# Kernel tuning notes

Hardware: AMD Instinct MI355X
Metric: run time of the kernel (lower is better)

## Reference

```python
import jax, jax.numpy as jnp
import numpy as np

B, S, C = 64, 2048, 128
P, Q = 4, 4


def setup_inputs() -> dict:
    key = jax.random.key(0)
    k1, k2, k3 = jax.random.split(key, 3)
    y = jax.random.normal(k1, (B, S, C), dtype=jnp.float32)
    # small positive coefficients keep the MA recurrence stable over S steps
    phi = 0.1 * jax.random.uniform(k2, (P,), dtype=jnp.float32)
    theta = 0.1 * jax.random.uniform(k3, (Q,), dtype=jnp.float32)
    sigma2 = jnp.ones((1,), dtype=jnp.float32)
    return {"y": y, "phi": phi, "theta": theta, "sigma2": sigma2}


def reference(y, phi, theta, sigma2):
    # ARIMA negative log-likelihood (arima_log_likelihood):
    #   e_t = y_t - sum_i phi_i * y_{t-i-1} - sum_j theta_j * e_{t-j-1}
    #   nll = -[ -0.5*S*log(2*pi*sigma2) - 0.5*sum(e^2)/sigma2 ]
    b, s, c = y.shape
    p = phi.shape[0]
    q = theta.shape[0]

    # AR part is a fixed causal convolution over the input -> precompute, vectorized.
    ypad = jnp.pad(y, ((0, 0), (p, 0), (0, 0)))  # zeros for t-i-1 < 0
    # lags[i, :, t, :] = y[:, t-i-1, :]   (zero when out of range)
    lags = jnp.stack([ypad[:, p - 1 - i: p - 1 - i + s, :] for i in range(p)], axis=0)
    z = y - jnp.einsum('i,ibsc->bsc', phi, lags)  # (B,S,C)

    # MA part is a true recurrence on the errors -> lax.scan over time.
    def step(carry, z_t):
        # carry: (q, B, C) = [e_{t-1}, e_{t-2}, ..., e_{t-q}] (most recent first)
        ma = jnp.einsum('j,jbc->bc', theta, carry)
        e_t = z_t - ma
        carry = jnp.concatenate([e_t[None], carry[:-1]], axis=0)
        return carry, e_t

    e0 = jnp.zeros((q, b, c), dtype=z.dtype)
    _, e = jax.lax.scan(step, e0, jnp.swapaxes(z, 0, 1))  # e: (S,B,C)

    ll = -0.5 * s * jnp.log(2.0 * jnp.pi * sigma2) - 0.5 * jnp.sum(e * e) / sigma2
    return -ll  # shape (1,)
```

## Files before the change

kernel.cpp:

```cpp
#include <hip/hip_runtime.h>
#include <math.h>

#define BB   64
#define SS   2048
#define CC   128
#define C4   (CC / 4)
#define LCH  64
#define NCH  (SS / LCH)
#define WARM 32
#define UNR  16
#define STEPS (WARM + LCH)
#define NBLK  (STEPS / UNR)
#define WBLK  (WARM / UNR)

#define ARIMA_BATCH(SRC, ACCT)                                            \
    _Pragma("unroll")                                                     \
    for (int j = 0; j < UNR; ++j) {                                       \
        _Pragma("unroll")                                                 \
        for (int k = 0; k < 4; ++k) {                                     \
            const float y0 = SRC[j][k];                                   \
            const float z  = y0 - p1*Y1[k] - p2*Y2[k] - p3*Y3[k] - p4*Y4[k]; \
            const float e0 = z  - q2*E2[k] - q3*E3[k] - q4*E4[k] - q1*E1[k]; \
            if (ACCT) acc[k] += e0 * e0;                                  \
            Y4[k] = Y3[k]; Y3[k] = Y2[k]; Y2[k] = Y1[k]; Y1[k] = y0;      \
            E4[k] = E3[k]; E3[k] = E2[k]; E2[k] = E1[k]; E1[k] = e0;      \
        }                                                                 \
    }

__global__ __launch_bounds__(64) void arima_main(
    const float4* __restrict__ yv,
    const float* __restrict__ phi,
    const float* __restrict__ theta,
    float* __restrict__ partials)
{
    const int bid  = blockIdx.x;
    const int lane = threadIdx.x;
    const int grp  = lane >> 5;
    const int ch   = lane & 31;
    const int b    = bid >> 4;
    const int chunk = ((bid & 15) << 1) | grp;

    const float p1 = phi[0],   p2 = phi[1],   p3 = phi[2],   p4 = phi[3];
    const float q1 = theta[0], q2 = theta[1], q3 = theta[2], q4 = theta[3];

    const float4* base = yv + (size_t)b * SS * C4 + ch;
    const int t0 = chunk * LCH - WARM;

    float Y1[4] = {0,0,0,0}, Y2[4] = {0,0,0,0}, Y3[4] = {0,0,0,0}, Y4[4] = {0,0,0,0};
    if (t0 >= 4) {
        float4 v;
        v = base[(size_t)(t0-1) * C4]; Y1[0]=v.x; Y1[1]=v.y; Y1[2]=v.z; Y1[3]=v.w;
        v = base[(size_t)(t0-2) * C4]; Y2[0]=v.x; Y2[1]=v.y; Y2[2]=v.z; Y2[3]=v.w;
        v = base[(size_t)(t0-3) * C4]; Y3[0]=v.x; Y3[1]=v.y; Y3[2]=v.z; Y3[3]=v.w;
        v = base[(size_t)(t0-4) * C4]; Y4[0]=v.x; Y4[1]=v.y; Y4[2]=v.z; Y4[3]=v.w;
    }
    float E1[4] = {0,0,0,0}, E2[4] = {0,0,0,0}, E3[4] = {0,0,0,0}, E4[4] = {0,0,0,0};
    float acc[4] = {0,0,0,0};

    int tcur = t0;
    float cur[UNR][4];
#pragma unroll
    for (int j = 0; j < UNR; ++j) {
        const int t = tcur + j;
        float4 v = (t >= 0) ? base[(size_t)t * C4] : make_float4(0.f,0.f,0.f,0.f);
        cur[j][0]=v.x; cur[j][1]=v.y; cur[j][2]=v.z; cur[j][3]=v.w;
    }
    tcur += UNR;

    for (int blk = 0; blk < NBLK - 1; ++blk) {
        float nxt[UNR][4];
#pragma unroll
        for (int j = 0; j < UNR; ++j) {
            const int t = tcur + j;
            float4 v = (t >= 0) ? base[(size_t)t * C4] : make_float4(0.f,0.f,0.f,0.f);
            nxt[j][0]=v.x; nxt[j][1]=v.y; nxt[j][2]=v.z; nxt[j][3]=v.w;
        }
        tcur += UNR;
        const bool acct = (blk >= WBLK);
        ARIMA_BATCH(cur, acct)
#pragma unroll
        for (int j = 0; j < UNR; ++j) {
            cur[j][0]=nxt[j][0]; cur[j][1]=nxt[j][1];
            cur[j][2]=nxt[j][2]; cur[j][3]=nxt[j][3];
        }
    }
    ARIMA_BATCH(cur, true)

    float a = acc[0] + acc[1] + acc[2] + acc[3];
#pragma unroll
    for (int off = 32; off > 0; off >>= 1)
        a += __shfl_down(a, off, 64);
    if (lane == 0) partials[bid] = a;
}

__global__ __launch_bounds__(256) void arima_final(
    const float* __restrict__ partials,
    const float* __restrict__ sigma2,
    float* __restrict__ out)
{
    float v = 0.f;
#pragma unroll
    for (int i = 0; i < 4; ++i)
        v += partials[threadIdx.x + 256 * i];
#pragma unroll
    for (int off = 32; off > 0; off >>= 1)
        v += __shfl_down(v, off, 64);
    __shared__ float sw[4];
    if ((threadIdx.x & 63) == 0) sw[threadIdx.x >> 6] = v;
    __syncthreads();
    if (threadIdx.x == 0) {
        const float tot = sw[0] + sw[1] + sw[2] + sw[3];
        const float s2 = sigma2[0];
        out[0] = 0.5f * (float)SS * logf(2.0f * 3.14159265358979323846f * s2)
               + 0.5f * tot / s2;
    }
}

extern "C" void kernel_launch(void* const* d_in, const int* in_sizes, int n_in,
                              void* d_out, int out_size, void* d_ws, size_t ws_size,
                              hipStream_t stream) {
    const float4* yv    = (const float4*)d_in[0];
    const float* phi    = (const float*)d_in[1];
    const float* theta  = (const float*)d_in[2];
    const float* sigma2 = (const float*)d_in[3];
    float* out      = (float*)d_out;
    float* partials = (float*)d_ws;

    arima_main<<<BB * NCH / 2, 64, 0, stream>>>(yv, phi, theta, partials);
    arima_final<<<1, 256, 0, stream>>>(partials, sigma2, out);
}
```

Baseline: 101.9 us.

## Lengthen time chunks, halve channels per thread, fuse final reduction via atomics

Time chunks grow from 64 to 128 steps, and each thread now handles 2 channels with float2 loads instead of 4 with float4, keeping the same total thread count. Each wave covers one (batch, chunk) pair in 256-thread blocks, which cuts the share of redundant warm-up steps. The separate final-reduction kernel is removed: blocks atomically add their sums into a global accumulator, and the last block to finish computes the output, with a memset clearing the counters before launch. The trade-off is a longer serial recurrence per thread with only two independent chains to hide latency. The float atomic accumulation also makes the summation order nondeterministic.

```diff
diff --git a/kernel.cpp b/kernel.cpp
--- a/kernel.cpp
+++ b/kernel.cpp
@@ -4,128 +4,122 @@
 #define BB   64
 #define SS   2048
 #define CC   128
-#define C4   (CC / 4)
-#define LCH  64
+#define C2   (CC / 2)
+#define LCH  128
 #define NCH  (SS / LCH)
 #define WARM 32
 #define UNR  16
 #define STEPS (WARM + LCH)
 #define NBLK  (STEPS / UNR)
 #define WBLK  (WARM / UNR)
+#define GRID  (BB * NCH / 4)
 
-#define ARIMA_BATCH(SRC, ACCT)                                            \
-    _Pragma("unroll")                                                     \
-    for (int j = 0; j < UNR; ++j) {                                       \
-        _Pragma("unroll")                                                 \
-        for (int k = 0; k < 4; ++k) {                                     \
-            const float y0 = SRC[j][k];                                   \
+#define ARIMA_BATCH(SRC, ACCT)                                               \
+    _Pragma("unroll")                                                        \
+    for (int j = 0; j < UNR; ++j) {                                          \
+        _Pragma("unroll")                                                    \
+        for (int k = 0; k < 2; ++k) {                                        \
+            const float y0 = SRC[j][k];                                      \
             const float z  = y0 - p1*Y1[k] - p2*Y2[k] - p3*Y3[k] - p4*Y4[k]; \
             const float e0 = z  - q2*E2[k] - q3*E3[k] - q4*E4[k] - q1*E1[k]; \
-            if (ACCT) acc[k] += e0 * e0;                                  \
-            Y4[k] = Y3[k]; Y3[k] = Y2[k]; Y2[k] = Y1[k]; Y1[k] = y0;      \
-            E4[k] = E3[k]; E3[k] = E2[k]; E2[k] = E1[k]; E1[k] = e0;      \
-        }                                                                 \
+            if (ACCT) acc[k] += e0 * e0;                                     \
+            Y4[k] = Y3[k]; Y3[k] = Y2[k]; Y2[k] = Y1[k]; Y1[k] = y0;         \
+            E4[k] = E3[k]; E3[k] = E2[k]; E2[k] = E1[k]; E1[k] = e0;         \
+        }                                                                    \
     }
 
-__global__ __launch_bounds__(64) void arima_main(
-    const float4* __restrict__ yv,
+__global__ __launch_bounds__(256) void arima_fused(
+    const float2* __restrict__ yv,
     const float* __restrict__ phi,
     const float* __restrict__ theta,
-    float* __restrict__ partials)
+    const float* __restrict__ sigma2,
+    float* __restrict__ out,
+    float* __restrict__ gsum,
+    unsigned int* __restrict__ gcnt)
 {
-    const int bid  = blockIdx.x;
-    const int lane = threadIdx.x;
-    const int grp  = lane >> 5;
-    const int ch   = lane & 31;
-    const int b    = bid >> 4;
-    const int chunk = ((bid & 15) << 1) | grp;
+    const int grp  = threadIdx.x >> 6;
+    const int lane = threadIdx.x & 63;
+    const int gid  = (blockIdx.x << 2) | grp;
+    const int b    = gid >> 4;
+    const int chunk = gid & 15;
 
     const float p1 = phi[0],   p2 = phi[1],   p3 = phi[2],   p4 = phi[3];
     const float q1 = theta[0], q2 = theta[1], q3 = theta[2], q4 = theta[3];
 
-    const float4* base = yv + (size_t)b * SS * C4 + ch;
+    const float2* base = yv + (size_t)b * SS * C2 + lane;
     const int t0 = chunk * LCH - WARM;
 
-    float Y1[4] = {0,0,0,0}, Y2[4] = {0,0,0,0}, Y3[4] = {0,0,0,0}, Y4[4] = {0,0,0,0};
-    if (t0 >= 4) {
-        float4 v;
-        v = base[(size_t)(t0-1) * C4]; Y1[0]=v.x; Y1[1]=v.y; Y1[2]=v.z; Y1[3]=v.w;
-        v = base[(size_t)(t0-2) * C4]; Y2[0]=v.x; Y2[1]=v.y; Y2[2]=v.z; Y2[3]=v.w;
-        v = base[(size_t)(t0-3) * C4]; Y3[0]=v.x; Y3[1]=v.y; Y3[2]=v.z; Y3[3]=v.w;
-        v = base[(size_t)(t0-4) * C4]; Y4[0]=v.x; Y4[1]=v.y; Y4[2]=v.z; Y4[3]=v.w;
+    float Y1[2] = {0,0}, Y2[2] = {0,0}, Y3[2] = {0,0}, Y4[2] = {0,0};
+    if (chunk) {
+        float2 v;
+        v = base[(size_t)(t0-1) * C2]; Y1[0]=v.x; Y1[1]=v.y;
+        v = base[(size_t)(t0-2) * C2]; Y2[0]=v.x; Y2[1]=v.y;
+        v = base[(size_t)(t0-3) * C2]; Y3[0]=v.x; Y3[1]=v.y;
+        v = base[(size_t)(t0-4) * C2]; Y4[0]=v.x; Y4[1]=v.y;
     }
-    float E1[4] = {0,0,0,0}, E2[4] = {0,0,0,0}, E3[4] = {0,0,0,0}, E4[4] = {0,0,0,0};
-    float acc[4] = {0,0,0,0};
+    float E1[2] = {0,0}, E2[2] = {0,0}, E3[2] = {0,0}, E4[2] = {0,0};
+    float acc[2] = {0,0};
 
     int tcur = t0;
-    float cur[UNR][4];
+    float cur[UNR][2];
 #pragma unroll
     for (int j = 0; j < UNR; ++j) {
         const int t = tcur + j;
-        float4 v = (t >= 0) ? base[(size_t)t * C4] : make_float4(0.f,0.f,0.f,0.f);
-        cur[j][0]=v.x; cur[j][1]=v.y; cur[j][2]=v.z; cur[j][3]=v.w;
+        float2 v = (t >= 0) ? base[(size_t)t * C2] : make_float2(0.f, 0.f);
+        cur[j][0] = v.x; cur[j][1] = v.y;
     }
     tcur += UNR;
 
     for (int blk = 0; blk < NBLK - 1; ++blk) {
-        float nxt[UNR][4];
+        float nxt[UNR][2];
 #pragma unroll
         for (int j = 0; j < UNR; ++j) {
             const int t = tcur + j;
-            float4 v = (t >= 0) ? base[(size_t)t * C4] : make_float4(0.f,0.f,0.f,0.f);
-            nxt[j][0]=v.x; nxt[j][1]=v.y; nxt[j][2]=v.z; nxt[j][3]=v.w;
+            float2 v = (t >= 0) ? base[(size_t)t * C2] : make_float2(0.f, 0.f);
+            nxt[j][0] = v.x; nxt[j][1] = v.y;
         }
         tcur += UNR;
         const bool acct = (blk >= WBLK);
         ARIMA_BATCH(cur, acct)
 #pragma unroll
-        for (int j = 0; j < UNR; ++j) {
-            cur[j][0]=nxt[j][0]; cur[j][1]=nxt[j][1];
-            cur[j][2]=nxt[j][2]; cur[j][3]=nxt[j][3];
-        }
+        for (int j = 0; j < UNR; ++j) { cur[j][0] = nxt[j][0]; cur[j][1] = nxt[j][1]; }
     }
     ARIMA_BATCH(cur, true)
 
-    float a = acc[0] + acc[1] + acc[2] + acc[3];
+    float a = acc[0] + acc[1];
 #pragma unroll
     for (int off = 32; off > 0; off >>= 1)
         a += __shfl_down(a, off, 64);
-    if (lane == 0) partials[bid] = a;
-}
+    __shared__ float sw[4];
+    if (lane == 0) sw[grp] = a;
+    __syncthreads();
 
-__global__ __launch_bounds__(256) void arima_final(
-    const float* __restrict__ partials,
-    const float* __restrict__ sigma2,
-    float* __restrict__ out)
-{
-    float v = 0.f;
-#pragma unroll
-    for (int i = 0; i < 4; ++i)
-        v += partials[threadIdx.x + 256 * i];
-#pragma unroll
-    for (int off = 32; off > 0; off >>= 1)
-        v += __shfl_down(v, off, 64);
-    __shared__ float sw[4];
-    if ((threadIdx.x & 63) == 0) sw[threadIdx.x >> 6] = v;
-    __syncthreads();
     if (threadIdx.x == 0) {
-        const float tot = sw[0] + sw[1] + sw[2] + sw[3];
-        const float s2 = sigma2[0];
-        out[0] = 0.5f * (float)SS * logf(2.0f * 3.14159265358979323846f * s2)
-               + 0.5f * tot / s2;
+        const float blocksum = sw[0] + sw[1] + sw[2] + sw[3];
+        atomicAdd(gsum, blocksum);
+        __threadfence();
+        const unsigned int old = atomicAdd(gcnt, 1u);
+        if (old == GRID - 1) {
+            const float tot = atomicAdd(gsum, 0.0f);
+            const float s2  = sigma2[0];
+            out[0] = 0.5f * (float)SS * logf(2.0f * 3.14159265358979323846f * s2)
+                   + 0.5f * tot / s2;
+        }
     }
 }
 
 extern "C" void kernel_launch(void* const* d_in, const int* in_sizes, int n_in,
                               void* d_out, int out_size, void* d_ws, size_t ws_size,
                               hipStream_t stream) {
-    const float4* yv    = (const float4*)d_in[0];
+    const float2* yv    = (const float2*)d_in[0];
     const float* phi    = (const float*)d_in[1];
     const float* theta  = (const float*)d_in[2];
     const float* sigma2 = (const float*)d_in[3];
-    float* out      = (float*)d_out;
-    float* partials = (float*)d_ws;
+    float* out = (float*)d_out;
 
-    arima_main<<<BB * NCH / 2, 64, 0, stream>>>(yv, phi, theta, partials);
-    arima_final<<<1, 256, 0, stream>>>(partials, sigma2, out);
+    float* gsum        = (float*)d_ws;
+    unsigned int* gcnt = (unsigned int*)((char*)d_ws + 8);
+
+    hipMemsetAsync(d_ws, 0, 16, stream);
+    arima_fused<<<GRID, 256, 0, stream>>>(yv, phi, theta, sigma2, out, gsum, gcnt);
 }
```

New measurement: 105.2 us. 3.3% more time.
